# Kernel tuning notes

Measured on AMD Instinct MI355X. Metric: run time of the kernel, lower is better.

The kernel has to match this reference:

```python
import jax, jax.numpy as jnp
import numpy as np
import math

IN_CH = 512
KEY_SIZE = 512
VALUE_SIZE = 512
B, T = 8, 2048


def setup_inputs() -> dict:
    key = jax.random.key(0)
    ks = jax.random.split(key, 7)
    s = 1.0 / math.sqrt(IN_CH)
    return {
        "x": jax.random.normal(ks[0], (B, T, IN_CH), dtype=jnp.float32),
        "Wq": jax.random.uniform(ks[1], (IN_CH, KEY_SIZE), jnp.float32, -s, s),
        "bq": jax.random.uniform(ks[2], (KEY_SIZE,), jnp.float32, -s, s),
        "Wk": jax.random.uniform(ks[3], (IN_CH, KEY_SIZE), jnp.float32, -s, s),
        "bk": jax.random.uniform(ks[4], (KEY_SIZE,), jnp.float32, -s, s),
        "Wv": jax.random.uniform(ks[5], (IN_CH, VALUE_SIZE), jnp.float32, -s, s),
        "bv": jax.random.uniform(ks[6], (VALUE_SIZE,), jnp.float32, -s, s),
    }


def reference(x, Wq, bq, Wk, bk, Wv, bv):
    # Projections (single head)
    q = jnp.einsum('btc,ck->btk', x, Wq) + bq  # [B,T,K]
    k = jnp.einsum('btc,ck->btk', x, Wk) + bk  # [B,T,K]
    v = jnp.einsum('btc,cv->btv', x, Wv) + bv  # [B,T,V]
    # Full score matrix, causal mask (strictly upper triangle masked: col > row)
    scores = jnp.einsum('bqk,btk->bqt', q, k)  # [B,T,T]
    t = scores.shape[1]
    causal = jnp.arange(t)[None, :] > jnp.arange(t)[:, None]  # True where future
    scores = jnp.where(causal[None], -jnp.inf, scores)
    attn = jax.nn.softmax(scores / math.sqrt(KEY_SIZE), axis=2)
    out = jnp.einsum('bqt,btv->bqv', attn, v)  # [B,T,V]
    return jnp.concatenate((x, out), axis=2)  # [B,T,C+V]
```

## Files before the change

### kernel.cpp

```cpp
#include <hip/hip_runtime.h>


#define DEV __device__ __forceinline__

typedef unsigned short u16;
typedef unsigned int u32;
typedef __attribute__((ext_vector_type(8))) short short8;
typedef __attribute__((ext_vector_type(4))) float float4v;

DEV u16 f2bf(float f) {
    u32 u = __float_as_uint(f);
    return (u16)((u + 0x7FFFu + ((u >> 16) & 1u)) >> 16);
}
DEV float bf2f(u16 h) { return __uint_as_float(((u32)h) << 16); }

DEV float4v mfma16(short8 a, short8 b, float4v c) {
    return __builtin_amdgcn_mfma_f32_16x16x32_bf16(a, b, c, 0, 0, 0);
}

#define GLD16(gptr, lptr)                                                     \
    __builtin_amdgcn_global_load_lds(                                         \
        (const __attribute__((address_space(1))) void*)(gptr),                \
        (__attribute__((address_space(3))) void*)(lptr), 16, 0, 0)

__global__ void prep_k(const void* __restrict__ x,
                       const void* __restrict__ Wq, const void* __restrict__ Wk,
                       const void* __restrict__ Wv, const void* __restrict__ bq,
                       const void* __restrict__ bk, const void* __restrict__ bv,
                       int* __restrict__ flag, u16* __restrict__ xb,
                       void* __restrict__ out, u16* __restrict__ Wt,
                       u16* __restrict__ bbuf) {
    int lane = threadIdx.x & 63;
    u32 ws = ((const u32*)x)[lane * 16];
    int e = (ws >> 7) & 0xFF;
    unsigned long long m = __ballot(e >= 0x60 && e <= 0x90);
    int isbf = (__popcll(m) > 32) ? 1 : 0;

    int bid = blockIdx.x;
    if (bid == 0 && threadIdx.x == 0) flag[0] = isbf;

    if (bid < 4096) {
        int i0 = (bid * 256 + threadIdx.x) * 8;
        int row = i0 >> 9, col = i0 & 511;
        if (isbf) {
            uint4 v = *(const uint4*)((const u16*)x + i0);
            *(uint4*)&xb[i0] = v;
            *(uint4*)((u16*)out + (size_t)row * 1024 + col) = v;
        } else {
            const float* xf = (const float*)x;
            float4 f0 = *(const float4*)(xf + i0);
            float4 f1 = *(const float4*)(xf + i0 + 4);
            union { u16 us[8]; uint4 v; } pk;
            pk.us[0] = f2bf(f0.x); pk.us[1] = f2bf(f0.y);
            pk.us[2] = f2bf(f0.z); pk.us[3] = f2bf(f0.w);
            pk.us[4] = f2bf(f1.x); pk.us[5] = f2bf(f1.y);
            pk.us[6] = f2bf(f1.z); pk.us[7] = f2bf(f1.w);
            *(uint4*)&xb[i0] = pk.v;
            float* o = (float*)out + (size_t)row * 1024 + col;
            *(float4*)o = f0; *(float4*)(o + 4) = f1;
        }
        return;
    }

    int rem = bid - 4096;
    int z = rem / 1026;
    int ix = rem - z * 1026;
    if (ix >= 1024) {
        int i = (ix - 1024) * 256 + threadIdx.x;
        const void* s = (z == 0) ? bq : ((z == 1) ? bk : bv);
        bbuf[z * 512 + i] = isbf ? ((const u16*)s)[i]
                                 : f2bf(((const float*)s)[i]);
        return;
    }
    const void* W = (z == 0) ? Wq : ((z == 1) ? Wk : Wv);
    int flat = ix * 256 + threadIdx.x;
    int n = flat >> 9, k = flat & 511;
    u16 v = isbf ? ((const u16*)W)[k * 512 + n]
                 : f2bf(((const float*)W)[k * 512 + n]);
    Wt[z * 262144 + flat] = v;
}

#define PWB(N)                                                                \
    do {                                                                      \
        asm volatile("s_waitcnt vmcnt(" #N ")" ::: "memory");                 \
        __builtin_amdgcn_s_barrier();                                         \
        asm volatile("" ::: "memory");                                        \
    } while (0)

__global__ __launch_bounds__(256) void proj_k(
        const u16* __restrict__ x, const u16* __restrict__ Wt,
        const u16* __restrict__ bb,
        u16* __restrict__ Qo, u16* __restrict__ Ko, u16* __restrict__ Vt_out) {
    int z = blockIdx.z;
    const u16* Wz = Wt + z * 262144;
    const u16* bias = bb + z * 512;
    int mBase = blockIdx.x * 128;
    int nBase = blockIdx.y * 128;

    __shared__ __attribute__((aligned(16))) u16 Xs[2][128 * 32];
    __shared__ __attribute__((aligned(16))) u16 Ws[2][128 * 32];

    int tid = threadIdx.x;
    int w = tid >> 6, lane = tid & 63, quad = lane >> 4, l16 = lane & 15;
    int wr = (w >> 1) * 64, wc = (w & 1) * 64;

#define PISSUE(bi, k0)                                                        \
    { _Pragma("unroll")                                                       \
      for (int gg = 0; gg < 2; gg++) {                                        \
        int g = w * 2 + gg;                                                   \
        int row = g * 16 + (lane >> 2);                                       \
        int c8 = (lane & 3) ^ ((row >> 1) & 3);                               \
        GLD16(&x [(size_t)(mBase + row) * 512 + (k0) + c8 * 8], &Xs[bi][g * 512]); \
        GLD16(&Wz[(size_t)(nBase + row) * 512 + (k0) + c8 * 8], &Ws[bi][g * 512]); \
      } }

    PISSUE(0, 0)
    PISSUE(1, 32)

    float4v acc[4][4] = {};

    #pragma unroll 2
    for (int t = 0; t < 16; t++) {
        int bi = t & 1;
        if (t < 15) { PWB(4); } else { PWB(0); }

        short8 a[4], b[4];
        #pragma unroll
        for (int mt = 0; mt < 4; mt++) {
            int rr = wr + mt * 16 + l16;
            a[mt] = *(const short8*)&Xs[bi][rr * 32 + ((quad ^ ((rr >> 1) & 3)) * 8)];
        }
        #pragma unroll
        for (int nt = 0; nt < 4; nt++) {
            int rr = wc + nt * 16 + l16;
            b[nt] = *(const short8*)&Ws[bi][rr * 32 + ((quad ^ ((rr >> 1) & 3)) * 8)];
        }
        #pragma unroll
        for (int mt = 0; mt < 4; mt++)
            #pragma unroll
            for (int nt = 0; nt < 4; nt++)
                acc[mt][nt] = mfma16(a[mt], b[nt], acc[mt][nt]);

        if (t < 14) {
            asm volatile("s_waitcnt lgkmcnt(0)" ::: "memory");
            __builtin_amdgcn_s_barrier();
            asm volatile("" ::: "memory");
            PISSUE(bi, (t + 2) * 32)
        }
    }

    #pragma unroll
    for (int nt = 0; nt < 4; nt++) {
        int n = nBase + wc + nt * 16 + l16;
        float bval = bf2f(bias[n]);
        #pragma unroll
        for (int mt = 0; mt < 4; mt++) {
            int m0 = mBase + wr + mt * 16 + quad * 4;
            float4v v = acc[mt][nt];
            if (z == 2) {
                int bbi = m0 >> 11, tt = m0 & 2047;
                u16 t0 = f2bf(v[0] + bval), t1 = f2bf(v[1] + bval);
                u16 t2 = f2bf(v[2] + bval), t3 = f2bf(v[3] + bval);
                uint2 pk = make_uint2((u32)t0 | ((u32)t1 << 16), (u32)t2 | ((u32)t3 << 16));
                *(uint2*)&Vt_out[((size_t)bbi * 512 + n) * 2048 + tt] = pk;
            } else {
                u16* dst = (z == 0) ? Qo : Ko;
                #pragma unroll
                for (int r = 0; r < 4; r++)
                    dst[(size_t)(m0 + r) * 512 + n] = f2bf(v[r] + bval);
            }
        }
    }
}


#define LOADK(dst, kB, half)                                                  \
    { _Pragma("unroll")                                                       \
      for (int j = 0; j < 8; j++) {                                           \
        int row2 = 2 * (j * 4 + w);                                           \
        int row = row2 + (lane >> 5);                                         \
        int col8 = lane & 31;                                                 \
        GLD16(&Kb[(size_t)((kB) + row) * 512 + (half) * 256 +                 \
                  ((col8 ^ (row & 7)) << 3)], &dst[row2 * 256]);              \
      } }

#define LOADV(dst, kB, half)                                                  \
    { _Pragma("unroll")                                                       \
      for (int j = 0; j < 8; j++) {                                           \
        int blk8 = 8 * (j * 4 + w);                                           \
        int dl = blk8 + (lane >> 3);                                          \
        int col8 = lane & 7;                                                  \
        GLD16(&Vb[(size_t)((half) * 256 + dl) * 2048 + (kB) +                 \
                  ((col8 ^ (dl & 7)) << 3)], &dst[blk8 * 64]);                \
      } }

#define SSTEP(buf, h)                                                         \
    { _Pragma("unroll")                                                       \
      for (int kk = 0; kk < 8; kk++) {                                        \
        _Pragma("unroll")                                                     \
        for (int nt = 0; nt < 4; nt++) {                                      \
          short8 bf = *(const short8*)&buf[(nt * 16 + l16) * 256 +            \
                                           (((kk * 4 + quad) ^ sw) << 3)];    \
          accS[nt] = mfma16(qf[(h) * 8 + kk], bf, accS[nt]);                  \
        } } }

#define PVSTEP(buf, accO)                                                     \
    { _Pragma("unroll")                                                       \
      for (int kk = 0; kk < 2; kk++) {                                        \
        _Pragma("unroll")                                                     \
        for (int dt = 0; dt < 4; dt++) {                                      \
          int rowv = w * 64 + dt * 16 + l16;                                  \
          short8 bf = *(const short8*)&buf[rowv * 64 +                        \
                                           (((kk * 4 + quad) ^ sw) << 3)];    \
          _Pragma("unroll")                                                   \
          for (int mt = 0; mt < 4; mt++)                                      \
            accO[dt][mt] = mfma16(pf[mt][kk], bf, accO[dt][mt]);              \
        } } }

__global__ __launch_bounds__(256, 1) void attn_k(
        const u16* __restrict__ Q, const u16* __restrict__ K,
        const u16* __restrict__ Vt, const int* __restrict__ flag,
        void* __restrict__ out, u16* __restrict__ Opart,
        float2* __restrict__ ml, int dosplit) {
    int blk = blockIdx.x;
    int b, qt, h, kt0, kt1;
    if (dosplit) {
        qt = (blk < 256) ? (31 - (blk >> 4)) : ((blk - 256) >> 4);
        h  = (blk >> 3) & 1;
        b  = blk & 7;
        int n = qt + 1, mid = n >> 1;
        kt0 = h ? mid : 0;
        kt1 = h ? n : mid;
    } else {
        qt = 31 - (blk >> 3);
        h  = 0;
        b  = blk & 7;
        kt0 = 0; kt1 = qt + 1;
    }
    int q0 = qt * 64;
    int isbf = flag[0];

    __shared__ __attribute__((aligned(16))) u16 KV0[16384];
    __shared__ __attribute__((aligned(16))) u16 KV1[16384];
    __shared__ __attribute__((aligned(16))) u16 Ps[4096];
    __shared__ float al_s[64];
    __shared__ float il_s[64];
    __shared__ int skip_s[4];

    int tid = threadIdx.x;
    int w = tid >> 6, lane = tid & 63, quad = lane >> 4, l16 = lane & 15;
    int sw = l16 & 7;

    const u16* Qb = Q  + (size_t)b * 2048 * 512;
    const u16* Kb = K  + (size_t)b * 2048 * 512;
    const u16* Vb = Vt + (size_t)b * 512 * 2048;

    if (kt0 < kt1) LOADK(KV0, kt0 * 64, 0);

    short8 qf[16];
    {
        const u16* Qrow = &Qb[(size_t)(q0 + w * 16 + l16) * 512];
        #pragma unroll
        for (int g = 0; g < 16; g++)
            qf[g] = *(const short8*)&Qrow[g * 32 + quad * 8];
    }

    float4v accO0[4][4] = {};
    float4v accO1[4][4] = {};
    float4v accS[4] = {};
    short8 pf[4][2];
    float mrow[4] = {-1e30f, -1e30f, -1e30f, -1e30f};
    float lrow[4] = {0.f, 0.f, 0.f, 0.f};
    const float scale = 0.044194173824159216f;

    __syncthreads();

    for (int kt = kt0; kt < kt1; kt++) {
        int kB = kt * 64;

        LOADK(KV1, kB, 1);
        SSTEP(KV0, 0);
        __syncthreads();

        LOADV(KV0, kB, 0);
        SSTEP(KV1, 1);
        {
            int diag = (kt == qt);
            float pv[4][4], mx4[4], alpha[4];
            #pragma unroll
            for (int r = 0; r < 4; r++) {
                float mx = -1e30f;
                #pragma unroll
                for (int nt = 0; nt < 4; nt++) {
                    float sv = accS[nt][r] * scale;
                    if (diag && (nt * 16 + l16 > w * 16 + quad * 4 + r)) sv = -1e30f;
                    pv[nt][r] = sv;
                    mx = fmaxf(mx, sv);
                }
                mx = fmaxf(mx, __shfl_xor(mx, 1));
                mx = fmaxf(mx, __shfl_xor(mx, 2));
                mx = fmaxf(mx, __shfl_xor(mx, 4));
                mx = fmaxf(mx, __shfl_xor(mx, 8));
                mx4[r] = mx;
            }
            int small = (mx4[0] - mrow[0] <= 8.f) && (mx4[1] - mrow[1] <= 8.f) &&
                        (mx4[2] - mrow[2] <= 8.f) && (mx4[3] - mrow[3] <= 8.f);
            int wskip = __all(small) ? 1 : 0;
            if (lane == 0) skip_s[w] = wskip;
            #pragma unroll
            for (int r = 0; r < 4; r++) {
                float mnew = wskip ? mrow[r] : fmaxf(mrow[r], mx4[r]);
                float a = wskip ? 1.0f : __expf(mrow[r] - mnew);
                float sum = 0.f;
                #pragma unroll
                for (int nt = 0; nt < 4; nt++) {
                    pv[nt][r] = __expf(pv[nt][r] - mnew);
                    sum += pv[nt][r];
                }
                sum += __shfl_xor(sum, 1);
                sum += __shfl_xor(sum, 2);
                sum += __shfl_xor(sum, 4);
                sum += __shfl_xor(sum, 8);
                lrow[r] = lrow[r] * a + sum;
                mrow[r] = mnew;
                alpha[r] = a;
            }
            #pragma unroll
            for (int nt = 0; nt < 4; nt++)
                #pragma unroll
                for (int r = 0; r < 4; r++)
                    Ps[(w * 16 + quad * 4 + r) * 64 + nt * 16 + l16] = f2bf(pv[nt][r]);
            #pragma unroll
            for (int r = 0; r < 4; r++) al_s[w * 16 + quad * 4 + r] = alpha[r];
            #pragma unroll
            for (int nt = 0; nt < 4; nt++) accS[nt] = (float4v){0.f, 0.f, 0.f, 0.f};
        }
        __syncthreads();

        LOADV(KV1, kB, 1);
        {
            #pragma unroll
            for (int mt = 0; mt < 4; mt++)
                #pragma unroll
                for (int kk = 0; kk < 2; kk++)
                    pf[mt][kk] = *(const short8*)&Ps[(mt * 16 + l16) * 64 +
                                                     kk * 32 + quad * 8];
            int bskip = skip_s[0] & skip_s[1] & skip_s[2] & skip_s[3];
            if (!bskip) {
                float alf[4][4];
                #pragma unroll
                for (int mt = 0; mt < 4; mt++)
                    #pragma unroll
                    for (int r = 0; r < 4; r++)
                        alf[mt][r] = al_s[mt * 16 + quad * 4 + r];
                #pragma unroll
                for (int dt = 0; dt < 4; dt++)
                    #pragma unroll
                    for (int mt = 0; mt < 4; mt++)
                        #pragma unroll
                        for (int r = 0; r < 4; r++) {
                            accO0[dt][mt][r] *= alf[mt][r];
                            accO1[dt][mt][r] *= alf[mt][r];
                        }
            }
        }
        PVSTEP(KV0, accO0);
        __syncthreads();

        if (kt + 1 < kt1) LOADK(KV0, kB + 64, 0);
        PVSTEP(KV1, accO1);
        __syncthreads();
    }

    if (dosplit) {
        if (l16 == 0) {
            #pragma unroll
            for (int r = 0; r < 4; r++) {
                int grow = b * 2048 + q0 + w * 16 + quad * 4 + r;
                ml[h * 16384 + grow] = make_float2(mrow[r], lrow[r]);
            }
        }
        #pragma unroll
        for (int dt = 0; dt < 4; dt++) {
            int dg = w * 64 + dt * 16 + l16;
            #pragma unroll
            for (int mt = 0; mt < 4; mt++)
                #pragma unroll
                for (int r = 0; r < 4; r++) {
                    int grow = b * 2048 + q0 + mt * 16 + quad * 4 + r;
                    size_t base = ((size_t)h * 16384 + grow) * 512;
                    Opart[base + dg]       = f2bf(accO0[dt][mt][r]);
                    Opart[base + dg + 256] = f2bf(accO1[dt][mt][r]);
                }
        }
    } else {
        #pragma unroll
        for (int r = 0; r < 4; r++) il_s[w * 16 + quad * 4 + r] = 1.0f / lrow[r];
        __syncthreads();
        float invl[4][4];
        #pragma unroll
        for (int mt = 0; mt < 4; mt++)
            #pragma unroll
            for (int r = 0; r < 4; r++) invl[mt][r] = il_s[mt * 16 + quad * 4 + r];
        u16*   o16 = (u16*)out;
        float* o32 = (float*)out;
        #pragma unroll
        for (int dt = 0; dt < 4; dt++) {
            int dg0 = 512 + w * 64 + dt * 16 + l16;
            #pragma unroll
            for (int mt = 0; mt < 4; mt++)
                #pragma unroll
                for (int r = 0; r < 4; r++) {
                    int rowg = q0 + mt * 16 + quad * 4 + r;
                    size_t base = ((size_t)b * 2048 + rowg) * 1024;
                    float v0 = accO0[dt][mt][r] * invl[mt][r];
                    float v1 = accO1[dt][mt][r] * invl[mt][r];
                    if (isbf) {
                        o16[base + dg0]       = f2bf(v0);
                        o16[base + dg0 + 256] = f2bf(v1);
                    } else {
                        o32[base + dg0]       = v0;
                        o32[base + dg0 + 256] = v1;
                    }
                }
        }
    }
}

__global__ __launch_bounds__(256) void combine_k(
        const u16* __restrict__ Opart, const float2* __restrict__ ml,
        const int* __restrict__ flag, void* __restrict__ out) {
    int tid = threadIdx.x;
    int grow = blockIdx.x * 4 + (tid >> 6);
    int d0 = (tid & 63) * 8;
    float2 ml0 = ml[grow], ml1 = ml[16384 + grow];
    float m = fmaxf(ml0.x, ml1.x);
    float a0 = __expf(ml0.x - m), a1 = __expf(ml1.x - m);
    float il = 1.0f / (ml0.y * a0 + ml1.y * a1);
    a0 *= il; a1 *= il;
    uint4 v0 = *(const uint4*)&Opart[(size_t)grow * 512 + d0];
    uint4 v1 = *(const uint4*)&Opart[(size_t)(16384 + grow) * 512 + d0];
    const u16* u0 = (const u16*)&v0;
    const u16* u1 = (const u16*)&v1;
    float res[8];
    #pragma unroll
    for (int i = 0; i < 8; i++)
        res[i] = bf2f(u0[i]) * a0 + bf2f(u1[i]) * a1;
    size_t base = (size_t)grow * 1024 + 512 + d0;
    if (flag[0]) {
        union { u16 us[8]; uint4 v; } pk;
        #pragma unroll
        for (int i = 0; i < 8; i++) pk.us[i] = f2bf(res[i]);
        *(uint4*)((u16*)out + base) = pk.v;
    } else {
        float* o = (float*)out + base;
        *(float4*)o = make_float4(res[0], res[1], res[2], res[3]);
        *(float4*)(o + 4) = make_float4(res[4], res[5], res[6], res[7]);
    }
}

extern "C" void kernel_launch(void* const* d_in, const int* in_sizes, int n_in,
                              void* d_out, int out_size, void* d_ws, size_t ws_size,
                              hipStream_t stream) {
    const void* x  = d_in[0];
    const void* Wq = d_in[1];
    const void* bq = d_in[2];
    const void* Wk = d_in[3];
    const void* bk = d_in[4];
    const void* Wv = d_in[5];
    const void* bv = d_in[6];

    u16* base = (u16*)d_ws;
    int* flag = (int*)base;
    u16* Wt   = base + 8;
    u16* bb   = Wt + 786432;
    u16* xb   = bb + 1544;
    u16* Qw   = xb + 8388608;
    u16* Kw   = Qw + 8388608;
    u16* Vtw  = Kw + 8388608;
    u16* Opart = Vtw + 8388608;
    float2* mlb = (float2*)(Opart + 16777216);

    size_t need = ((size_t)(Opart - base) + 16777216) * 2 + 262144;
    int dosplit = (ws_size >= need) ? 1 : 0;

    hipLaunchKernelGGL(prep_k, dim3(7174), dim3(256), 0, stream,
                       x, Wq, Wk, Wv, bq, bk, bv, flag, xb, d_out, Wt, bb);
    hipLaunchKernelGGL(proj_k, dim3(128, 4, 3), dim3(256), 0, stream, xb, Wt, bb, Qw, Kw, Vtw);
    if (dosplit) {
        hipLaunchKernelGGL(attn_k, dim3(512), dim3(256), 0, stream,
                           Qw, Kw, Vtw, flag, d_out, Opart, mlb, 1);
        hipLaunchKernelGGL(combine_k, dim3(4096), dim3(256), 0, stream,
                           Opart, mlb, flag, d_out);
    } else {
        hipLaunchKernelGGL(attn_k, dim3(256), dim3(256), 0, stream,
                           Qw, Kw, Vtw, flag, d_out, Opart, mlb, 0);
    }
}
```

Baseline: 280.3 us.

## Tile weight transpose through LDS and stage projection epilogue for coalesced stores

The weight transpose in prep_k now moves 64x64 tiles through shared memory, so both the reads and the writes are vectorized and coalesced, replacing the old scattered per-element strided reads. The block count shrinks to match. The proj_k epilogue now writes bias-added bf16 results into a swizzled per-wave LDS staging area and then emits 16-byte coalesced global stores for Q, K and the transposed V, instead of 2-byte scattered writes. The cost is an extra LDS round trip plus a barrier, and the LDS buffers are merged so the staging area can reuse them.

```diff
diff --git a/kernel.cpp b/kernel.cpp
--- a/kernel.cpp
+++ b/kernel.cpp
@@ -30,17 +30,19 @@
                        int* __restrict__ flag, u16* __restrict__ xb,
                        void* __restrict__ out, u16* __restrict__ Wt,
                        u16* __restrict__ bbuf) {
-    int lane = threadIdx.x & 63;
+    __shared__ __attribute__((aligned(16))) u16 T[64 * 80];
+    int tid = threadIdx.x;
+    int lane = tid & 63;
     u32 ws = ((const u32*)x)[lane * 16];
     int e = (ws >> 7) & 0xFF;
     unsigned long long m = __ballot(e >= 0x60 && e <= 0x90);
     int isbf = (__popcll(m) > 32) ? 1 : 0;
 
     int bid = blockIdx.x;
-    if (bid == 0 && threadIdx.x == 0) flag[0] = isbf;
+    if (bid == 0 && tid == 0) flag[0] = isbf;
 
     if (bid < 4096) {
-        int i0 = (bid * 256 + threadIdx.x) * 8;
+        int i0 = (bid * 256 + tid) * 8;
         int row = i0 >> 9, col = i0 & 511;
         if (isbf) {
             uint4 v = *(const uint4*)((const u16*)x + i0);
@@ -62,22 +64,51 @@
         return;
     }
 
-    int rem = bid - 4096;
-    int z = rem / 1026;
-    int ix = rem - z * 1026;
-    if (ix >= 1024) {
-        int i = (ix - 1024) * 256 + threadIdx.x;
+    if (bid >= 4288) {
+        int j = bid - 4288;
+        int z = j >> 1;
+        int i = (j & 1) * 256 + tid;
         const void* s = (z == 0) ? bq : ((z == 1) ? bk : bv);
         bbuf[z * 512 + i] = isbf ? ((const u16*)s)[i]
                                  : f2bf(((const float*)s)[i]);
         return;
     }
+
+    int widx = bid - 4096;
+    int z = widx >> 6;
+    int t64 = widx & 63;
+    int k0 = (t64 >> 3) * 64, n0 = (t64 & 7) * 64;
     const void* W = (z == 0) ? Wq : ((z == 1) ? Wk : Wv);
-    int flat = ix * 256 + threadIdx.x;
-    int n = flat >> 9, k = flat & 511;
-    u16 v = isbf ? ((const u16*)W)[k * 512 + n]
-                 : f2bf(((const float*)W)[k * 512 + n]);
-    Wt[z * 262144 + flat] = v;
+    if (isbf) {
+        #pragma unroll
+        for (int p = 0; p < 2; p++) {
+            int idx = p * 256 + tid;
+            int k = idx >> 3, c8 = idx & 7;
+            short8 v = *(const short8*)((const u16*)W + (size_t)(k0 + k) * 512 + n0 + c8 * 8);
+            #pragma unroll
+            for (int j = 0; j < 8; j++)
+                T[(c8 * 8 + j) * 80 + k] = (u16)v[j];
+        }
+    } else {
+        #pragma unroll
+        for (int p = 0; p < 4; p++) {
+            int idx = p * 256 + tid;
+            int k = idx >> 4, c4 = idx & 15;
+            float4 f = *(const float4*)((const float*)W + (size_t)(k0 + k) * 512 + n0 + c4 * 4);
+            T[(c4 * 4 + 0) * 80 + k] = f2bf(f.x);
+            T[(c4 * 4 + 1) * 80 + k] = f2bf(f.y);
+            T[(c4 * 4 + 2) * 80 + k] = f2bf(f.z);
+            T[(c4 * 4 + 3) * 80 + k] = f2bf(f.w);
+        }
+    }
+    __syncthreads();
+    #pragma unroll
+    for (int p = 0; p < 2; p++) {
+        int idx = p * 256 + tid;
+        int n = idx >> 3, c8 = idx & 7;
+        short8 o = *(const short8*)&T[n * 80 + c8 * 8];
+        *(uint4*)&Wt[z * 262144 + (size_t)(n0 + n) * 512 + k0 + c8 * 8] = *(uint4*)&o;
+    }
 }
 
 #define PWB(N)                                                                \
@@ -97,8 +128,9 @@
     int mBase = blockIdx.x * 128;
     int nBase = blockIdx.y * 128;
 
-    __shared__ __attribute__((aligned(16))) u16 Xs[2][128 * 32];
-    __shared__ __attribute__((aligned(16))) u16 Ws[2][128 * 32];
+    __shared__ __attribute__((aligned(16))) u16 LDSBUF[16384];
+#define XSB(bi) (&LDSBUF[(bi) * 4096])
+#define WSB(bi) (&LDSBUF[8192 + (bi) * 4096])
 
     int tid = threadIdx.x;
     int w = tid >> 6, lane = tid & 63, quad = lane >> 4, l16 = lane & 15;
@@ -110,8 +142,8 @@
         int g = w * 2 + gg;                                                   \
         int row = g * 16 + (lane >> 2);                                       \
         int c8 = (lane & 3) ^ ((row >> 1) & 3);                               \
-        GLD16(&x [(size_t)(mBase + row) * 512 + (k0) + c8 * 8], &Xs[bi][g * 512]); \
-        GLD16(&Wz[(size_t)(nBase + row) * 512 + (k0) + c8 * 8], &Ws[bi][g * 512]); \
+        GLD16(&x [(size_t)(mBase + row) * 512 + (k0) + c8 * 8], &XSB(bi)[g * 512]); \
+        GLD16(&Wz[(size_t)(nBase + row) * 512 + (k0) + c8 * 8], &WSB(bi)[g * 512]); \
       } }
 
     PISSUE(0, 0)
@@ -128,12 +160,12 @@
         #pragma unroll
         for (int mt = 0; mt < 4; mt++) {
             int rr = wr + mt * 16 + l16;
-            a[mt] = *(const short8*)&Xs[bi][rr * 32 + ((quad ^ ((rr >> 1) & 3)) * 8)];
+            a[mt] = *(const short8*)&XSB(bi)[rr * 32 + ((quad ^ ((rr >> 1) & 3)) * 8)];
         }
         #pragma unroll
         for (int nt = 0; nt < 4; nt++) {
             int rr = wc + nt * 16 + l16;
-            b[nt] = *(const short8*)&Ws[bi][rr * 32 + ((quad ^ ((rr >> 1) & 3)) * 8)];
+            b[nt] = *(const short8*)&WSB(bi)[rr * 32 + ((quad ^ ((rr >> 1) & 3)) * 8)];
         }
         #pragma unroll
         for (int mt = 0; mt < 4; mt++)
@@ -149,28 +181,69 @@
         }
     }
 
-    #pragma unroll
-    for (int nt = 0; nt < 4; nt++) {
-        int n = nBase + wc + nt * 16 + l16;
-        float bval = bf2f(bias[n]);
-        #pragma unroll
-        for (int mt = 0; mt < 4; mt++) {
-            int m0 = mBase + wr + mt * 16 + quad * 4;
-            float4v v = acc[mt][nt];
-            if (z == 2) {
-                int bbi = m0 >> 11, tt = m0 & 2047;
+    __syncthreads();
+    u16* stg = &LDSBUF[w * 4096];
+
+    if (z == 2) {
+        #pragma unroll
+        for (int nt = 0; nt < 4; nt++) {
+            int rl = nt * 16 + l16;
+            float bval = bf2f(bias[nBase + wc + rl]);
+            int rx = rl & 7;
+            #pragma unroll
+            for (int mt = 0; mt < 4; mt++) {
+                int g  = mt * 2 + (quad >> 1);
+                int b0 = (quad & 1) * 4;
+                float4v v = acc[mt][nt];
                 u16 t0 = f2bf(v[0] + bval), t1 = f2bf(v[1] + bval);
                 u16 t2 = f2bf(v[2] + bval), t3 = f2bf(v[3] + bval);
-                uint2 pk = make_uint2((u32)t0 | ((u32)t1 << 16), (u32)t2 | ((u32)t3 << 16));
-                *(uint2*)&Vt_out[((size_t)bbi * 512 + n) * 2048 + tt] = pk;
-            } else {
-                u16* dst = (z == 0) ? Qo : Ko;
-                #pragma unroll
-                for (int r = 0; r < 4; r++)
-                    dst[(size_t)(m0 + r) * 512 + n] = f2bf(v[r] + bval);
+                uint2 pk = make_uint2((u32)t0 | ((u32)t1 << 16),
+                                      (u32)t2 | ((u32)t3 << 16));
+                *(uint2*)&stg[rl * 64 + ((g ^ rx) << 3) + b0] = pk;
             }
         }
-    }
+        asm volatile("s_waitcnt lgkmcnt(0)" ::: "memory");
+        int bbi = (mBase + wr) >> 11;
+        int tt0 = (mBase + wr) & 2047;
+        #pragma unroll
+        for (int i = 0; i < 8; i++) {
+            int rl = i * 8 + (lane >> 3);
+            int c8 = lane & 7;
+            short8 s = *(const short8*)&stg[rl * 64 + ((c8 ^ (rl & 7)) << 3)];
+            *(uint4*)&Vt_out[((size_t)bbi * 512 + nBase + wc + rl) * 2048 +
+                             tt0 + c8 * 8] = *(uint4*)&s;
+        }
+    } else {
+        u16* dst = (z == 0) ? Qo : Ko;
+        #pragma unroll
+        for (int nt = 0; nt < 4; nt++) {
+            int cl = nt * 16 + l16;
+            float bval = bf2f(bias[nBase + wc + cl]);
+            int g = nt * 2 + (l16 >> 3);
+            int b = l16 & 7;
+            #pragma unroll
+            for (int mt = 0; mt < 4; mt++) {
+                float4v v = acc[mt][nt];
+                #pragma unroll
+                for (int r = 0; r < 4; r++) {
+                    int rl = mt * 16 + quad * 4 + r;
+                    stg[rl * 64 + ((g ^ (rl & 7)) << 3) + b] = f2bf(v[r] + bval);
+                }
+            }
+        }
+        asm volatile("s_waitcnt lgkmcnt(0)" ::: "memory");
+        #pragma unroll
+        for (int i = 0; i < 8; i++) {
+            int rl = i * 8 + (lane >> 3);
+            int c8 = lane & 7;
+            short8 s = *(const short8*)&stg[rl * 64 + ((c8 ^ (rl & 7)) << 3)];
+            *(uint4*)&dst[(size_t)(mBase + wr + rl) * 512 +
+                          nBase + wc + c8 * 8] = *(uint4*)&s;
+        }
+    }
+#undef PISSUE
+#undef XSB
+#undef WSB
 }
 
 
@@ -484,7 +557,7 @@
     size_t need = ((size_t)(Opart - base) + 16777216) * 2 + 262144;
     int dosplit = (ws_size >= need) ? 1 : 0;
 
-    hipLaunchKernelGGL(prep_k, dim3(7174), dim3(256), 0, stream,
+    hipLaunchKernelGGL(prep_k, dim3(4294), dim3(256), 0, stream,
                        x, Wq, Wk, Wv, bq, bk, bv, flag, xb, d_out, Wt, bb);
     hipLaunchKernelGGL(proj_k, dim3(128, 4, 3), dim3(256), 0, stream, xb, Wt, bb, Qw, Kw, Vtw);
     if (dosplit) {
```

Result: faster. 266.1 us (-5.0%).
